# Kernel optimization log

Measured on AMD Instinct MI355X. Metric: run time of the kernel, lower is better.

Reference implementation:

```python
import jax, jax.numpy as jnp
import numpy as np

K_NB = 16
HID = 64
CIN = 128
EPS = 1e-5


def knn_idx(q, t, k):
    # q [B,N,3] queries, t [B,M,3] targets -> idx [B,N,k] into targets
    d = (jnp.sum(q * q, -1)[:, :, None] + jnp.sum(t * t, -1)[:, None, :]
         - 2.0 * jnp.einsum('bnd,bmd->bnm', q, t))
    _, idx = jax.lax.top_k(-d, k)
    return idx


def gather(feat, idx):
    # feat [B,C,M], idx [B,N,K] -> [B,C,N,K]
    return jax.vmap(lambda f, i: f[:, i])(feat, idx)


def conv1x1(x, W, b):
    # x [B,C,N,K], W [O,C], b [O]
    return jnp.einsum('oc,bcnk->bonk', W, x) + b[None, :, None, None]


def group_norm(x, gamma, beta, groups):
    B, C, N, K = x.shape
    xg = x.reshape(B, groups, C // groups, N, K)
    m = xg.mean(axis=(2, 3, 4), keepdims=True)
    v = xg.var(axis=(2, 3, 4), keepdims=True)
    xg = (xg - m) / jnp.sqrt(v + EPS)
    x = xg.reshape(B, C, N, K)
    return x * gamma[None, :, None, None] + beta[None, :, None, None]


def leaky(x):
    return jnp.where(x >= 0, x, 0.1 * x)


def setup_inputs() -> dict:
    key = jax.random.key(0)
    ks = jax.random.split(key, 20)
    B, N = 2, 4096
    d = {
        'xyz0': jax.random.normal(ks[0], (B, 3, N), jnp.float32),
        'xyz1': jax.random.normal(ks[1], (B, 3, N), jnp.float32),
        'state': jax.random.normal(ks[2], (B, HID, N), jnp.float32),
        'corr0': jax.random.normal(ks[3], (B, HID, N), jnp.float32),
        'feat0': jax.random.normal(ks[4], (B, CIN, N), jnp.float32),
        'feat1': jax.random.normal(ks[5], (B, CIN, N), jnp.float32),
        'flow0': jax.random.normal(ks[6], (B, 3, N), jnp.float32),
        # flow_layer: SetConv(3, [64,64]) -> convs take 3+3=6 then 64 in-chans
        'fw1': jax.random.normal(ks[7], (64, 6), jnp.float32) * 0.05,
        'fb1': jnp.zeros((64,), jnp.float32),
        'fg1': jnp.ones((64,), jnp.float32),
        'fbe1': jnp.zeros((64,), jnp.float32),
        'fw2': jax.random.normal(ks[8], (64, 64), jnp.float32) * 0.05,
        'fb2': jnp.zeros((64,), jnp.float32),
        'fg2': jnp.ones((64,), jnp.float32),
        'fbe2': jnp.zeros((64,), jnp.float32),
        # GRU gates: SetConv in_feat = hid(64)+(hid+64=128)=192, +3 = 195 -> 64, no act
        'wz': jax.random.normal(ks[9], (HID, 195), jnp.float32) * 0.05,
        'bz': jnp.zeros((HID,), jnp.float32),
        'wr': jax.random.normal(ks[10], (HID, 195), jnp.float32) * 0.05,
        'br': jnp.zeros((HID,), jnp.float32),
        'wq': jax.random.normal(ks[11], (HID, 195), jnp.float32) * 0.05,
        'bq': jnp.zeros((HID,), jnp.float32),
        # interp weight_net: 2*128+3=259 -> 128 -> 64
        'wa1': jax.random.normal(ks[12], (CIN, 2 * CIN + 3), jnp.float32) * 0.05,
        'ba1': jnp.zeros((CIN,), jnp.float32),
        'wa2': jax.random.normal(ks[13], (HID, CIN), jnp.float32) * 0.05,
        'ba2': jnp.zeros((HID,), jnp.float32),
    }
    return d


def reference(xyz0, xyz1, state, corr0, feat0, feat1, flow0,
              fw1, fb1, fg1, fbe1, fw2, fb2, fg2, fbe2,
              wz, bz, wr, br, wq, bq, wa1, ba1, wa2, ba2):
    xyz0_t = xyz0.transpose(0, 2, 1)  # [B,N,3]
    xyz1_t = xyz1.transpose(0, 2, 1)

    # ---- flow_layer: SetConv (KNN, N==npoint so new_xyz = xyz0) ----
    idx0 = knn_idx(xyz0_t, xyz0_t, K_NB)              # [B,N,K]
    gxyz0 = gather(xyz0, idx0) - xyz0[:, :, :, None]  # [B,3,N,K]
    h = jnp.concatenate([gather(flow0, idx0), gxyz0], axis=1)  # [B,6,N,K]
    h = leaky(group_norm(conv1x1(h, fw1, fb1), fg1, fbe1, 64 // 16))
    h = leaky(group_norm(conv1x1(h, fw2, fb2), fg2, fbe2, 64 // 16))
    flow_feat = h.max(axis=3)  # [B,64,N]

    # ---- iter_layer: SetGRU over xyz0 neighbors ----
    feat_g = jnp.concatenate([corr0, flow_feat], axis=1)  # [B,128,N]

    def gate(f, W, b):
        g = jnp.concatenate([gather(f, idx0), gxyz0], axis=1)
        return conv1x1(g, W, b).max(axis=3)  # [B,64,N]

    hid_in = jnp.concatenate([feat_g, state], axis=1)  # [B,192,N]
    z = jax.nn.sigmoid(gate(hid_in, wz, bz))
    r = jax.nn.sigmoid(gate(hid_in, wr, br))
    q = jnp.tanh(gate(jnp.concatenate([feat_g, r * state], axis=1), wq, bq))
    next_state = (1.0 - z) * state + z * q  # [B,64,N]

    # ---- align_layer: SetInterp (queries xyz1, targets xyz0) ----
    idx1 = knn_idx(xyz1_t, xyz0_t, K_NB)
    gv = gather(next_state, idx1)                        # [B,64,N,K]
    gx = gather(xyz0, idx1) - xyz1[:, :, :, None]        # [B,3,N,K]
    gf = jnp.concatenate([
        gather(feat0, idx1),
        jnp.broadcast_to(feat1[:, :, :, None], feat1.shape + (K_NB,))], axis=1)
    w = conv1x1(jnp.concatenate([gf, gx], axis=1), wa1, ba1)
    w = conv1x1(leaky(w), wa2, ba2)
    w = jax.nn.softmax(w, axis=3)
    return jnp.sum(gv * w, axis=3)  # [B,64,N]
```

## Files before the change

### kernel.cpp

```cpp
#include <hip/hip_runtime.h>

#define B_SZ 2

__device__ __forceinline__ int rfl(int x) { return __builtin_amdgcn_readfirstlane(x); }
__device__ __forceinline__ float leaky(float v) { return v >= 0.f ? v : 0.1f * v; }

__launch_bounds__(256)
__global__ void pack_kernel(const float* __restrict__ xyz, float4* __restrict__ out, int N)
{
  int b = blockIdx.y;
  int i = blockIdx.x * 256 + threadIdx.x;
  if (i >= N) return;
  const float* p = xyz + (size_t)b * 3 * N;
  float x = p[i], y = p[N + i], z = p[2 * N + i];
  out[(size_t)b * N + i] = make_float4(x, y, z, x * x + y * y + z * z);
}

__device__ __forceinline__ void sort64(float& d, int& i, int lane)
{
#pragma unroll
  for (int k = 2; k <= 64; k <<= 1) {
#pragma unroll
    for (int j = k >> 1; j > 0; j >>= 1) {
      float od = __shfl_xor(d, j, 64);
      int   oi = __shfl_xor(i, j, 64);
      bool mineSmall = (d < od) || (d == od && i < oi);
      bool amLow = (lane & j) == 0;
      bool up = (lane & k) == 0;
      bool keepMine = (amLow == up) ? mineSmall : !mineSmall;
      if (!keepMine) { d = od; i = oi; }
    }
  }
}

__launch_bounds__(256)
__global__ void knn_wave_kernel(const float4* __restrict__ pk, const float* __restrict__ q,
                                int* __restrict__ idx, int N)
{
  __shared__ __align__(16) float4 ts[1024];
  __shared__ uint2 buf[4][256];
  const int b = blockIdx.y;
  const int lane = threadIdx.x & 63, wav = rfl(threadIdx.x >> 6);
  const int qi = blockIdx.x * 4 + wav;
  const float* qb = q + (size_t)b * 3 * N;
  const float qx = qb[qi], qy = qb[N + qi], qz = qb[2 * N + qi];
  const float qq = qx * qx + qy * qy + qz * qz;
  const float4* pb = pk + (size_t)b * N;

  float lmin = 3.0e38f;
  for (int ch = 0; ch < N; ch += 1024) {
    __syncthreads();
    for (int i = threadIdx.x; i < 1024; i += 256) ts[i] = pb[ch + i];
    __syncthreads();
#pragma unroll 4
    for (int sub = 0; sub < 16; ++sub) {
      float4 v = ts[sub * 64 + lane];
      float key = (qq + v.w) - 2.0f * (qx * v.x + qy * v.y + qz * v.z);
      lmin = fminf(lmin, key);
    }
  }
  float gm = fminf(lmin, __shfl_xor(lmin, 1, 64));
  gm = fminf(gm, __shfl_xor(gm, 2, 64));
  float t0 = gm;
  t0 = fmaxf(t0, __shfl_xor(t0, 4, 64));
  t0 = fmaxf(t0, __shfl_xor(t0, 8, 64));
  t0 = fmaxf(t0, __shfl_xor(t0, 16, 64));
  t0 = fmaxf(t0, __shfl_xor(t0, 32, 64));

  int cnt = 0;
  for (int ch = 0; ch < N; ch += 1024) {
    __syncthreads();
    for (int i = threadIdx.x; i < 1024; i += 256) ts[i] = pb[ch + i];
    __syncthreads();
    for (int sub = 0; sub < 16; ++sub) {
      float4 v = ts[sub * 64 + lane];
      float key = (qq + v.w) - 2.0f * (qx * v.x + qy * v.y + qz * v.z);
      bool qf = key <= t0;
      unsigned long long mask = __ballot(qf);
      if (mask) {
        unsigned lo = __builtin_amdgcn_mbcnt_lo((unsigned)mask, 0u);
        unsigned pre = __builtin_amdgcn_mbcnt_hi((unsigned)(mask >> 32), lo);
        if (qf) {
          unsigned slot = (unsigned)cnt + pre;
          if (slot < 256u)
            buf[wav][slot] = make_uint2(__float_as_uint(key), (unsigned)(ch + sub * 64 + lane));
        }
        cnt += (int)__popcll(mask);
      }
    }
  }
  int C = cnt < 256 ? cnt : 256;

  float kd = 3.0e38f; int ki = 0x7fffffff;
  if (lane < C) { uint2 u = buf[wav][lane]; kd = __uint_as_float(u.x); ki = (int)u.y; }
  sort64(kd, ki, lane);
  int consumed = C < 64 ? C : 64;
  while (consumed < C) {
    if (lane >= 16) {
      int j2 = consumed + (lane - 16);
      if (j2 < C) { uint2 u = buf[wav][j2]; kd = __uint_as_float(u.x); ki = (int)u.y; }
      else { kd = 3.0e38f; ki = 0x7fffffff; }
    }
    int t = C - consumed; consumed += (t < 48 ? t : 48);
    sort64(kd, ki, lane);
  }
  if (lane < 16) idx[((size_t)b * N + qi) * 16 + lane] = ki;
}

__launch_bounds__(256)
__global__ void prep_w_kernel(const float* __restrict__ wz, const float* __restrict__ wr,
    const float* __restrict__ wq, const float* __restrict__ wa1, const float* __restrict__ wa2,
    const float* __restrict__ bz, const float* __restrict__ br,
    float* __restrict__ WtZR, float* __restrict__ WtQ,
    float* __restrict__ WtU, float* __restrict__ WtV, float* __restrict__ WtA2,
    float* __restrict__ bZR)
{
  int job = blockIdx.x;
  int tid = threadIdx.x;
  if (job == 0) {
    for (int e = tid; e < 195 * 128; e += 256) {
      int k = e >> 7, o = e & 127;
      const float* w = (o < 64) ? wz : wr;
      WtZR[(size_t)k * 128 + o] = w[(size_t)(o & 63) * 195 + k];
    }
    if (tid < 128) bZR[tid] = (tid < 64) ? bz[tid] : br[tid - 64];
  } else if (job == 1) {
    for (int e = tid; e < 195 * 64; e += 256) {
      int k = e >> 6, o = e & 63;
      WtQ[(size_t)k * 64 + o] = wq[(size_t)o * 195 + k];
    }
  } else if (job == 2) {
    for (int e = tid; e < 131 * 128; e += 256) {
      int k = e >> 7, o = e & 127;
      int col = (k < 128) ? k : 256 + (k - 128);
      WtU[(size_t)k * 128 + o] = wa1[(size_t)o * 259 + col];
    }
  } else if (job == 3) {
    for (int e = tid; e < 131 * 128; e += 256) {
      int k = e >> 7, o = e & 127;
      float v = (k < 128) ? wa1[(size_t)o * 259 + 128 + k]
                          : -wa1[(size_t)o * 259 + 256 + (k - 128)];
      WtV[(size_t)k * 128 + o] = v;
    }
  } else {
    for (int e = tid; e < 128 * 64; e += 256) {
      int c = e >> 6, o = e & 63;
      WtA2[e] = wa2[(size_t)o * 128 + c];
    }
  }
}

#define KC 66
__launch_bounds__(256)
__global__ void projT_kernel(const float* __restrict__ Wt, int K, int WOUT,
    const float* __restrict__ bias, float* __restrict__ out,
    int N, int PN,
    const float* __restrict__ s0, int c0, int l0,
    const float* __restrict__ s1, int c1, int l1,
    const float* __restrict__ s2, int c2, int l2,
    const float* __restrict__ s3, int c3, int l3)
{
  __shared__ __align__(16) float Ws[KC][68];
  __shared__ __align__(16) float Xs[KC][68];
  const int n0 = blockIdx.x * 64;
  const int oo = blockIdx.y * 64;
  const int b = n0 / N;
  const int nn0 = n0 - b * N;
  const int tid = threadIdx.x;
  const int tx = tid & 15, ty = tid >> 4;
  const int o4 = tx * 4, n4 = ty * 4;
  float acc[4][4];
#pragma unroll
  for (int i = 0; i < 4; ++i)
#pragma unroll
    for (int j = 0; j < 4; ++j)
      acc[i][j] = bias ? bias[oo + o4 + j] : 0.0f;

  const int e01 = c0 + c1, e012 = c0 + c1 + c2;
  for (int k0 = 0; k0 < K; k0 += KC) {
    const int kc = min(KC, K - k0);
    __syncthreads();
    for (int e = tid; e < kc * 64; e += 256) {
      int k = e >> 6, o = e & 63;
      Ws[k][o] = Wt[(size_t)(k0 + k) * WOUT + oo + o];
    }
    for (int e = tid; e < kc * 64; e += 256) {
      int k = e >> 6, j = e & 63;
      int c = k0 + k;
      float v;
      if (c < c0)        v = l0 ? s0[(size_t)c * PN + n0 + j]
                                : s0[((size_t)b * c0 + c) * N + nn0 + j];
      else if (c < e01)  { int cc = c - c0;
                           v = l1 ? s1[(size_t)cc * PN + n0 + j]
                                  : s1[((size_t)b * c1 + cc) * N + nn0 + j]; }
      else if (c < e012) { int cc = c - e01;
                           v = l2 ? s2[(size_t)cc * PN + n0 + j]
                                  : s2[((size_t)b * c2 + cc) * N + nn0 + j]; }
      else               { int cc = c - e012;
                           v = l3 ? s3[(size_t)cc * PN + n0 + j]
                                  : s3[((size_t)b * c3 + cc) * N + nn0 + j]; }
      Xs[k][j] = v;
    }
    __syncthreads();
#pragma unroll 2
    for (int k = 0; k < kc; ++k) {
      float4 wv = *(const float4*)&Ws[k][o4];
      float4 xv = *(const float4*)&Xs[k][n4];
      acc[0][0] = fmaf(xv.x, wv.x, acc[0][0]); acc[0][1] = fmaf(xv.x, wv.y, acc[0][1]);
      acc[0][2] = fmaf(xv.x, wv.z, acc[0][2]); acc[0][3] = fmaf(xv.x, wv.w, acc[0][3]);
      acc[1][0] = fmaf(xv.y, wv.x, acc[1][0]); acc[1][1] = fmaf(xv.y, wv.y, acc[1][1]);
      acc[1][2] = fmaf(xv.y, wv.z, acc[1][2]); acc[1][3] = fmaf(xv.y, wv.w, acc[1][3]);
      acc[2][0] = fmaf(xv.z, wv.x, acc[2][0]); acc[2][1] = fmaf(xv.z, wv.y, acc[2][1]);
      acc[2][2] = fmaf(xv.z, wv.z, acc[2][2]); acc[2][3] = fmaf(xv.z, wv.w, acc[2][3]);
      acc[3][0] = fmaf(xv.w, wv.x, acc[3][0]); acc[3][1] = fmaf(xv.w, wv.y, acc[3][1]);
      acc[3][2] = fmaf(xv.w, wv.z, acc[3][2]); acc[3][3] = fmaf(xv.w, wv.w, acc[3][3]);
    }
  }
#pragma unroll
  for (int i = 0; i < 4; ++i) {
    float4 r = make_float4(acc[i][0], acc[i][1], acc[i][2], acc[i][3]);
    *(float4*)&out[(size_t)(n0 + n4 + i) * WOUT + oo + o4] = r;
  }
}

__launch_bounds__(256)
__global__ void projUV_kernel(const float* __restrict__ WtU, const float* __restrict__ WtV,
    const float* __restrict__ ba1, float* __restrict__ Uo, float* __restrict__ Vo,
    int N, int PN,
    const float* __restrict__ feat0, const float* __restrict__ feat1,
    const float* __restrict__ x0, const float* __restrict__ x1)
{
  __shared__ __align__(16) float Ws[KC][68];
  __shared__ __align__(16) float Xs[KC][68];
  const int z = blockIdx.z;
  const float* Wt = z ? WtV : WtU;
  const float* bias = z ? ba1 : 0;
  float* out = z ? Vo : Uo;
  const float* s0 = z ? feat1 : feat0;
  const float* s1 = z ? x1 : x0;
  const int K = 131, WOUT = 128, c0 = 128;
  const int n0 = blockIdx.x * 64;
  const int oo = blockIdx.y * 64;
  const int b = n0 / N;
  const int nn0 = n0 - b * N;
  const int tid = threadIdx.x;
  const int tx = tid & 15, ty = tid >> 4;
  const int o4 = tx * 4, n4 = ty * 4;
  float acc[4][4];
#pragma unroll
  for (int i = 0; i < 4; ++i)
#pragma unroll
    for (int j = 0; j < 4; ++j)
      acc[i][j] = bias ? bias[oo + o4 + j] : 0.0f;

  for (int k0 = 0; k0 < K; k0 += KC) {
    const int kc = min(KC, K - k0);
    __syncthreads();
    for (int e = tid; e < kc * 64; e += 256) {
      int k = e >> 6, o = e & 63;
      Ws[k][o] = Wt[(size_t)(k0 + k) * WOUT + oo + o];
    }
    for (int e = tid; e < kc * 64; e += 256) {
      int k = e >> 6, j = e & 63;
      int c = k0 + k;
      float v;
      if (c < c0) v = s0[((size_t)b * c0 + c) * N + nn0 + j];
      else        v = s1[((size_t)b * 3 + (c - c0)) * N + nn0 + j];
      Xs[k][j] = v;
    }
    __syncthreads();
#pragma unroll 2
    for (int k = 0; k < kc; ++k) {
      float4 wv = *(const float4*)&Ws[k][o4];
      float4 xv = *(const float4*)&Xs[k][n4];
      acc[0][0] = fmaf(xv.x, wv.x, acc[0][0]); acc[0][1] = fmaf(xv.x, wv.y, acc[0][1]);
      acc[0][2] = fmaf(xv.x, wv.z, acc[0][2]); acc[0][3] = fmaf(xv.x, wv.w, acc[0][3]);
      acc[1][0] = fmaf(xv.y, wv.x, acc[1][0]); acc[1][1] = fmaf(xv.y, wv.y, acc[1][1]);
      acc[1][2] = fmaf(xv.y, wv.z, acc[1][2]); acc[1][3] = fmaf(xv.y, wv.w, acc[1][3]);
      acc[2][0] = fmaf(xv.z, wv.x, acc[2][0]); acc[2][1] = fmaf(xv.z, wv.y, acc[2][1]);
      acc[2][2] = fmaf(xv.z, wv.z, acc[2][2]); acc[2][3] = fmaf(xv.z, wv.w, acc[2][3]);
      acc[3][0] = fmaf(xv.w, wv.x, acc[3][0]); acc[3][1] = fmaf(xv.w, wv.y, acc[3][1]);
      acc[3][2] = fmaf(xv.w, wv.z, acc[3][2]); acc[3][3] = fmaf(xv.w, wv.w, acc[3][3]);
    }
  }
#pragma unroll
  for (int i = 0; i < 4; ++i) {
    float4 r = make_float4(acc[i][0], acc[i][1], acc[i][2], acc[i][3]);
    *(float4*)&out[(size_t)(n0 + n4 + i) * WOUT + oo + o4] = r;
  }
}

__device__ __forceinline__ void seg_accumL(const float* __restrict__ p, int cnt,
    const float* __restrict__ WL, int sC, int sN, long n0, float acc[4])
{
#pragma unroll 4
  for (int c = 0; c < cnt; ++c) {
    float w = WL[c];
    const float* pp = p + (size_t)c * sC + (size_t)n0 * sN;
#pragma unroll
    for (int m = 0; m < 4; ++m)
      acc[m] = fmaf(w, pp[(size_t)m * sN], acc[m]);
  }
}

template<int WP>
__launch_bounds__(256)
__global__ void proj_kernel(
    const float* __restrict__ W0, const float* __restrict__ bias,
    float* __restrict__ out, int OUTS, int wld, int N,
    const float* __restrict__ s0, int c0, int w0,
    const float* __restrict__ s1, int c1, int w1)
{
  __shared__ float Wl[64 * WP];
  const int b = blockIdx.y;
  const int lane = threadIdx.x & 63;
  const int wav = rfl(threadIdx.x >> 6);
  for (int r = wav; r < 64; r += 4)
    for (int c = lane; c < c0; c += 64)
      Wl[r * WP + c] = W0[(size_t)r * wld + w0 + c];
  for (int r = wav; r < 64; r += 4)
    for (int c = lane; c < c1; c += 64)
      Wl[r * WP + c0 + c] = W0[(size_t)r * wld + w1 + c];
  __syncthreads();
  const long n0 = ((long)blockIdx.x * 4 + wav) * 4;
  float bv = bias ? bias[lane] : 0.0f;
  float acc[4] = {bv, bv, bv, bv};
  const float* WL = &Wl[lane * WP];
  seg_accumL(s0 + (size_t)b * c0 * N, c0, WL, N, 1, n0, acc);
  seg_accumL(s1 + (size_t)b * c1 * N, c1, WL + c0, N, 1, n0, acc);
#pragma unroll
  for (int m = 0; m < 4; ++m)
    out[((size_t)b * N + n0 + m) * OUTS + lane] = acc[m];
}

__launch_bounds__(256)
__global__ void gn1_stats_kernel(const float* __restrict__ G1, const float* __restrict__ xyz0,
    const float* __restrict__ fw1, const int* __restrict__ idx0,
    float* __restrict__ stats1, int N)
{
  __shared__ float red[4][4][2];
  int b = blockIdx.y;
  int lane = threadIdx.x & 63, wav = rfl(threadIdx.x >> 6);
  float wg0 = fw1[lane * 6 + 3], wg1 = fw1[lane * 6 + 4], wg2 = fw1[lane * 6 + 5];
  const float* xb = xyz0 + (size_t)b * 3 * N;
  float sum = 0.f, sq = 0.f;
  for (int n = blockIdx.x * 4 + wav; n < N; n += gridDim.x * 4) {
    const int* ip = idx0 + ((size_t)b * N + n) * 16;
    float bx = wg0 * xb[n] + wg1 * xb[N + n] + wg2 * xb[2 * N + n];
#pragma unroll
    for (int k = 0; k < 16; ++k) {
      int m = ip[k];
      float y = G1[((size_t)b * N + m) * 64 + lane] - bx;
      sum += y; sq += y * y;
    }
  }
#pragma unroll
  for (int off = 1; off < 16; off <<= 1) {
    sum += __shfl_xor(sum, off, 64);
    sq += __shfl_xor(sq, off, 64);
  }
  int g = lane >> 4;
  if ((lane & 15) == 0) { red[wav][g][0] = sum; red[wav][g][1] = sq; }
  __syncthreads();
  if (threadIdx.x < 8) {
    int gg = threadIdx.x >> 1, s = threadIdx.x & 1;
    float v = red[0][gg][s] + red[1][gg][s] + red[2][gg][s] + red[3][gg][s];
    atomicAdd(&stats1[(b * 4 + gg) * 2 + s], v);
  }
}

__launch_bounds__(256, 2)
__global__ void conv2_kernel(const float* __restrict__ G1, const float* __restrict__ xyz0,
    const float* __restrict__ fw1, const int* __restrict__ idx0,
    const float* __restrict__ fw2, const float* __restrict__ fb2,
    const float* __restrict__ fg1, const float* __restrict__ fbe1,
    const float* __restrict__ raw1, float cnt,
    float* __restrict__ y2max, float* __restrict__ y2min,
    float* __restrict__ stats2, int N)
{
  __shared__ __align__(16) float x2[4][16][64];
  __shared__ float red[4][4][2];
  const int b = blockIdx.y;
  const int lane = threadIdx.x & 63;
  const int wav = rfl(threadIdx.x >> 6);
  float4 w[16];
#pragma unroll
  for (int i = 0; i < 16; ++i) w[i] = *(const float4*)&fw2[lane * 64 + i * 4];
  float wg0 = fw1[lane * 6 + 3], wg1 = fw1[lane * 6 + 4], wg2 = fw1[lane * 6 + 5];
  const int g = lane >> 4;
  float s_ = raw1[(b * 4 + g) * 2], q_ = raw1[(b * 4 + g) * 2 + 1];
  float mu1 = s_ / cnt;
  float inv1 = rsqrtf(q_ / cnt - mu1 * mu1 + 1e-5f);
  float sc1 = fg1[lane] * inv1;
  float sh1 = fbe1[lane] - mu1 * sc1;
  float fb2l = fb2[lane];
  const float* xb = xyz0 + (size_t)b * 3 * N;
  float sum = 0.f, sq = 0.f;
  for (int n = blockIdx.x * 4 + wav; n < N; n += gridDim.x * 4) {
    const int* ip = idx0 + ((size_t)b * N + n) * 16;
    float bx = wg0 * xb[n] + wg1 * xb[N + n] + wg2 * xb[2 * N + n];
#pragma unroll
    for (int k = 0; k < 16; ++k) {
      int m = ip[k];
      float y = G1[((size_t)b * N + m) * 64 + lane] - bx;
      x2[wav][k][lane] = leaky(y * sc1 + sh1);
    }
    float acc[16];
#pragma unroll
    for (int k = 0; k < 16; ++k) acc[k] = fb2l;
#pragma unroll
    for (int c4 = 0; c4 < 16; ++c4) {
      float4 w4 = w[c4];
#pragma unroll
      for (int k = 0; k < 16; ++k) {
        float4 x4 = *(const float4*)&x2[wav][k][c4 * 4];
        acc[k] = fmaf(w4.x, x4.x, acc[k]);
        acc[k] = fmaf(w4.y, x4.y, acc[k]);
        acc[k] = fmaf(w4.z, x4.z, acc[k]);
        acc[k] = fmaf(w4.w, x4.w, acc[k]);
      }
    }
    float mx = -3.0e38f, mn = 3.0e38f;
#pragma unroll
    for (int k = 0; k < 16; ++k) {
      mx = fmaxf(mx, acc[k]); mn = fminf(mn, acc[k]);
      sum += acc[k]; sq += acc[k] * acc[k];
    }
    y2max[((size_t)b * N + n) * 64 + lane] = mx;
    y2min[((size_t)b * N + n) * 64 + lane] = mn;
  }
#pragma unroll
  for (int off = 1; off < 16; off <<= 1) {
    sum += __shfl_xor(sum, off, 64);
    sq += __shfl_xor(sq, off, 64);
  }
  if ((lane & 15) == 0) { red[wav][g][0] = sum; red[wav][g][1] = sq; }
  __syncthreads();
  if (threadIdx.x < 8) {
    int gg = threadIdx.x >> 1, s = threadIdx.x & 1;
    float v = red[0][gg][s] + red[1][gg][s] + red[2][gg][s] + red[3][gg][s];
    atomicAdd(&stats2[(b * 4 + gg) * 2 + s], v);
  }
}

__launch_bounds__(256)
__global__ void flow_feat_kernel(const float* __restrict__ y2max, const float* __restrict__ y2min,
    const float* __restrict__ raw2, float cnt,
    const float* __restrict__ fg2, const float* __restrict__ fbe2,
    float* __restrict__ ff_t, int N, int PN)
{
  size_t i = (size_t)blockIdx.x * blockDim.x + threadIdx.x;
  if (i >= (size_t)B_SZ * N * 64) return;
  int c = i & 63;
  size_t pn = i >> 6;
  int b = (int)(pn / N);
  int g = c >> 4;
  float s_ = raw2[(b * 4 + g) * 2], q_ = raw2[(b * 4 + g) * 2 + 1];
  float mu = s_ / cnt;
  float inv = rsqrtf(q_ / cnt - mu * mu + 1e-5f);
  float sc = fg2[c] * inv;
  float sh = fbe2[c] - mu * sc;
  float y = (sc >= 0.0f) ? y2max[i] : y2min[i];
  ff_t[(size_t)c * PN + pn] = leaky(y * sc + sh);
}

__launch_bounds__(256)
__global__ void gate_zr_kernel(const float* __restrict__ Szr,
    const float* __restrict__ wz, const float* __restrict__ wr,
    const float* __restrict__ xyz0, const float* __restrict__ state,
    const int* __restrict__ idx0,
    float* __restrict__ zo, float* __restrict__ rs_t, int N, int PN)
{
  int b = blockIdx.y;
  int lane = threadIdx.x & 63, wav = rfl(threadIdx.x >> 6);
  float wz0 = wz[lane * 195 + 192], wz1 = wz[lane * 195 + 193], wz2 = wz[lane * 195 + 194];
  float wr0 = wr[lane * 195 + 192], wr1 = wr[lane * 195 + 193], wr2 = wr[lane * 195 + 194];
  const float* xb = xyz0 + (size_t)b * 3 * N;
  for (int n = blockIdx.x * 4 + wav; n < N; n += gridDim.x * 4) {
    const int* ip = idx0 + ((size_t)b * N + n) * 16;
    float u0 = xb[n], u1 = xb[N + n], u2 = xb[2 * N + n];
    float xz = wz0 * u0 + wz1 * u1 + wz2 * u2;
    float xr = wr0 * u0 + wr1 * u1 + wr2 * u2;
    float mz = -3.0e38f, mr = -3.0e38f;
#pragma unroll
    for (int k = 0; k < 16; ++k) {
      size_t mo = ((size_t)b * N + ip[k]) * 128 + lane;
      mz = fmaxf(mz, Szr[mo]);
      mr = fmaxf(mr, Szr[mo + 64]);
    }
    size_t no = ((size_t)b * N + n) * 64 + lane;
    float z = 1.f / (1.f + expf(-(mz - xz)));
    float r = 1.f / (1.f + expf(-(mr - xr)));
    zo[no] = z;
    rs_t[(size_t)lane * PN + (size_t)b * N + n] = r * state[((size_t)b * 64 + lane) * N + n];
  }
}

__launch_bounds__(256)
__global__ void gate_q_ns_kernel(const float* __restrict__ Sq, const float* __restrict__ wq,
    const float* __restrict__ xyz0, const float* __restrict__ zo,
    const float* __restrict__ state, const int* __restrict__ idx0,
    float* __restrict__ ns, int N)
{
  int b = blockIdx.y;
  int lane = threadIdx.x & 63, wav = rfl(threadIdx.x >> 6);
  float wq0 = wq[lane * 195 + 192], wq1 = wq[lane * 195 + 193], wq2 = wq[lane * 195 + 194];
  const float* xb = xyz0 + (size_t)b * 3 * N;
  for (int n = blockIdx.x * 4 + wav; n < N; n += gridDim.x * 4) {
    const int* ip = idx0 + ((size_t)b * N + n) * 16;
    float xq = wq0 * xb[n] + wq1 * xb[N + n] + wq2 * xb[2 * N + n];
    float mq = -3.0e38f;
#pragma unroll
    for (int k = 0; k < 16; ++k)
      mq = fmaxf(mq, Sq[((size_t)b * N + ip[k]) * 64 + lane]);
    size_t no = ((size_t)b * N + n) * 64 + lane;
    float q = tanhf(mq - xq);
    float z = zo[no];
    float st = state[((size_t)b * 64 + lane) * N + n];
    ns[no] = (1.f - z) * st + z * q;
  }
}

__launch_bounds__(256, 2)
__global__ void align_kernel(const float* __restrict__ U, const float* __restrict__ V,
    const float* __restrict__ WtA2, const float* __restrict__ ba2,
    const float* __restrict__ ns, const int* __restrict__ idx1,
    float* __restrict__ out, int N)
{
  __shared__ __align__(16) float Xs[64][128];
  __shared__ __align__(16) float Ws[128][64];
  const int b = blockIdx.y;
  const int tid = threadIdx.x;
  const int lane = tid & 63;
  const int wav = rfl(tid >> 6);

  for (int e = tid; e < 2048; e += 256) {
    int c = e >> 4, o4 = (e & 15) << 2;
    *(float4*)&Ws[c][o4] = *(const float4*)&WtA2[(c << 6) + o4];
  }

  const int n = blockIdx.x * 4 + wav;
  int mkreg = 0;
  {
    const int* ip = idx1 + ((size_t)b * N + n) * 16;
    if (lane < 16) mkreg = ip[lane];
  }
  const int c4l = lane & 31;
  const int half = lane >> 5;
  float4 v4 = *(const float4*)&V[(((size_t)b * N + n) << 7) + (c4l << 2)];
  for (int k0 = 0; k0 < 16; k0 += 2) {
    int k = k0 + half;
    int m = __shfl(mkreg, k);
    float4 u4 = *(const float4*)&U[(((size_t)b * N + m) << 7) + (c4l << 2)];
    float4 xv;
    xv.x = leaky(u4.x + v4.x);
    xv.y = leaky(u4.y + v4.y);
    xv.z = leaky(u4.z + v4.z);
    xv.w = leaky(u4.w + v4.w);
    int row = (wav << 4) + k;
    *(float4*)&Xs[row][(c4l ^ (row & 7)) << 2] = xv;
  }
  __syncthreads();

  const int tx = tid & 15, ty = tid >> 4;
  const int o4 = tx << 2, r0 = ty << 2;
  float4 bav = *(const float4*)&ba2[o4];
  float acc[4][4];
#pragma unroll
  for (int i = 0; i < 4; ++i) {
    acc[i][0] = bav.x; acc[i][1] = bav.y; acc[i][2] = bav.z; acc[i][3] = bav.w;
  }
  for (int c4 = 0; c4 < 32; ++c4) {
    float4 wv0 = *(const float4*)&Ws[c4 * 4 + 0][o4];
    float4 wv1 = *(const float4*)&Ws[c4 * 4 + 1][o4];
    float4 wv2 = *(const float4*)&Ws[c4 * 4 + 2][o4];
    float4 wv3 = *(const float4*)&Ws[c4 * 4 + 3][o4];
#pragma unroll
    for (int i = 0; i < 4; ++i) {
      int row = r0 + i;
      float4 xv = *(const float4*)&Xs[row][(c4 ^ (row & 7)) << 2];
      acc[i][0] = fmaf(xv.x, wv0.x, acc[i][0]);
      acc[i][1] = fmaf(xv.x, wv0.y, acc[i][1]);
      acc[i][2] = fmaf(xv.x, wv0.z, acc[i][2]);
      acc[i][3] = fmaf(xv.x, wv0.w, acc[i][3]);
      acc[i][0] = fmaf(xv.y, wv1.x, acc[i][0]);
      acc[i][1] = fmaf(xv.y, wv1.y, acc[i][1]);
      acc[i][2] = fmaf(xv.y, wv1.z, acc[i][2]);
      acc[i][3] = fmaf(xv.y, wv1.w, acc[i][3]);
      acc[i][0] = fmaf(xv.z, wv2.x, acc[i][0]);
      acc[i][1] = fmaf(xv.z, wv2.y, acc[i][1]);
      acc[i][2] = fmaf(xv.z, wv2.z, acc[i][2]);
      acc[i][3] = fmaf(xv.z, wv2.w, acc[i][3]);
      acc[i][0] = fmaf(xv.w, wv3.x, acc[i][0]);
      acc[i][1] = fmaf(xv.w, wv3.y, acc[i][1]);
      acc[i][2] = fmaf(xv.w, wv3.z, acc[i][2]);
      acc[i][3] = fmaf(xv.w, wv3.w, acc[i][3]);
    }
  }

  float m_[4];
#pragma unroll
  for (int j = 0; j < 4; ++j) {
    float m = fmaxf(fmaxf(acc[0][j], acc[1][j]), fmaxf(acc[2][j], acc[3][j]));
    m = fmaxf(m, __shfl_xor(m, 16, 64));
    m = fmaxf(m, __shfl_xor(m, 32, 64));
    m_[j] = m;
  }
  float e_[4][4], s_[4];
#pragma unroll
  for (int j = 0; j < 4; ++j) {
    float s = 0.f;
#pragma unroll
    for (int i = 0; i < 4; ++i) { e_[i][j] = expf(acc[i][j] - m_[j]); s += e_[i][j]; }
    s += __shfl_xor(s, 16, 64);
    s += __shfl_xor(s, 32, 64);
    s_[j] = s;
  }
  float o_[4] = {0.f, 0.f, 0.f, 0.f};
#pragma unroll
  for (int i = 0; i < 4; ++i) {
    int k = (r0 + i) & 15;
    int m = __shfl(mkreg, k);
    float4 nsv = *(const float4*)&ns[(((size_t)b * N + m) << 6) + o4];
    o_[0] = fmaf(e_[i][0], nsv.x, o_[0]);
    o_[1] = fmaf(e_[i][1], nsv.y, o_[1]);
    o_[2] = fmaf(e_[i][2], nsv.z, o_[2]);
    o_[3] = fmaf(e_[i][3], nsv.w, o_[3]);
  }
#pragma unroll
  for (int j = 0; j < 4; ++j) {
    o_[j] += __shfl_xor(o_[j], 16, 64);
    o_[j] += __shfl_xor(o_[j], 32, 64);
  }
  if ((lane >> 4) == 0) {
#pragma unroll
    for (int j = 0; j < 4; ++j)
      out[((size_t)b * 64 + o4 + j) * N + n] = o_[j] / s_[j];
  }
}

extern "C" void kernel_launch(void* const* d_in, const int* in_sizes, int n_in,
                              void* d_out, int out_size, void* d_ws, size_t ws_size,
                              hipStream_t stream) {
  (void)n_in; (void)out_size; (void)ws_size;
  const float* xyz0 = (const float*)d_in[0];
  const float* xyz1 = (const float*)d_in[1];
  const float* state = (const float*)d_in[2];
  const float* corr0 = (const float*)d_in[3];
  const float* feat0 = (const float*)d_in[4];
  const float* feat1 = (const float*)d_in[5];
  const float* flow0 = (const float*)d_in[6];
  const float* fw1 = (const float*)d_in[7];
  const float* fb1 = (const float*)d_in[8];
  const float* fg1 = (const float*)d_in[9];
  const float* fbe1 = (const float*)d_in[10];
  const float* fw2 = (const float*)d_in[11];
  const float* fb2 = (const float*)d_in[12];
  const float* fg2 = (const float*)d_in[13];
  const float* fbe2 = (const float*)d_in[14];
  const float* wz = (const float*)d_in[15];
  const float* bz = (const float*)d_in[16];
  const float* wr = (const float*)d_in[17];
  const float* br = (const float*)d_in[18];
  const float* wq = (const float*)d_in[19];
  const float* bq = (const float*)d_in[20];
  const float* wa1 = (const float*)d_in[21];
  const float* ba1 = (const float*)d_in[22];
  const float* wa2 = (const float*)d_in[23];
  const float* ba2 = (const float*)d_in[24];
  float* out = (float*)d_out;

  const int N = in_sizes[0] / (3 * B_SZ);
  const int PN = B_SZ * N;
  char* wsb = (char*)d_ws;
  size_t off = 0;
  auto take = [&](size_t bytes) -> char* {
    char* p = wsb + off;
    off += (bytes + 255) & ~(size_t)255;
    return p;
  };
  float* U    = (float*)take((size_t)PN * 128 * 4);
  float* V    = (float*)take((size_t)PN * 128 * 4);
  float* Szr  = (float*)take((size_t)PN * 128 * 4);
  float4* pk0 = (float4*)take((size_t)PN * 4 * 4);
  int*   idx0 = (int*)  take((size_t)PN * 16 * 4);
  int*   idx1 = (int*)  take((size_t)PN * 16 * 4);
  float* G1   = (float*)take((size_t)PN * 64 * 4);
  float* y2mx = (float*)take((size_t)PN * 64 * 4);
  float* y2mn = (float*)take((size_t)PN * 64 * 4);
  float* ff_t = (float*)take((size_t)PN * 64 * 4);
  float* Sq   = (float*)take((size_t)PN * 64 * 4);
  float* zg   = (float*)take((size_t)PN * 64 * 4);
  float* rs_t = (float*)take((size_t)PN * 64 * 4);
  float* ns   = (float*)take((size_t)PN * 64 * 4);
  float* WtZR = (float*)take(195 * 128 * 4);
  float* WtQ  = (float*)take(195 * 64 * 4);
  float* WtU  = (float*)take(131 * 128 * 4);
  float* WtV  = (float*)take(131 * 128 * 4);
  float* WtA2 = (float*)take(128 * 64 * 4);
  float* bZR  = (float*)take(128 * 4);
  float* stats = (float*)take(256);
  float* raw1 = stats, *raw2 = stats + 16;

  const float cntv = 16.0f * N * 16.0f;

  hipMemsetAsync(raw1, 0, 32 * sizeof(float), stream);

  pack_kernel<<<dim3((N + 255) / 256, B_SZ), 256, 0, stream>>>(xyz0, pk0, N);
  prep_w_kernel<<<5, 256, 0, stream>>>(wz, wr, wq, wa1, wa2, bz, br,
      WtZR, WtQ, WtU, WtV, WtA2, bZR);
  knn_wave_kernel<<<dim3(N / 4, B_SZ), 256, 0, stream>>>(pk0, xyz0, idx0, N);
  knn_wave_kernel<<<dim3(N / 4, B_SZ), 256, 0, stream>>>(pk0, xyz1, idx1, N);

  proj_kernel<7><<<dim3(N / 16, B_SZ), 256, 0, stream>>>(
      fw1, fb1, G1, 64, 6, N, flow0, 3, 0, xyz0, 3, 3);

  gn1_stats_kernel<<<dim3(256, B_SZ), 256, 0, stream>>>(G1, xyz0, fw1, idx0, raw1, N);
  conv2_kernel<<<dim3(512, B_SZ), 256, 0, stream>>>(G1, xyz0, fw1, idx0, fw2, fb2, fg1, fbe1,
      raw1, cntv, y2mx, y2mn, raw2, N);
  flow_feat_kernel<<<dim3((unsigned)((size_t)PN * 64 / 256)), 256, 0, stream>>>(
      y2mx, y2mn, raw2, cntv, fg2, fbe2, ff_t, N, PN);

  projT_kernel<<<dim3(PN / 64, 2), 256, 0, stream>>>(WtZR, 195, 128, bZR, Szr, N, PN,
      corr0, 64, 0,  ff_t, 64, 1,  state, 64, 0,  xyz0, 3, 0);

  gate_zr_kernel<<<dim3(256, B_SZ), 256, 0, stream>>>(Szr, wz, wr, xyz0, state, idx0, zg, rs_t, N, PN);

  projT_kernel<<<dim3(PN / 64, 1), 256, 0, stream>>>(WtQ, 195, 64, bq, Sq, N, PN,
      corr0, 64, 0,  ff_t, 64, 1,  rs_t, 64, 1,  xyz0, 3, 0);

  gate_q_ns_kernel<<<dim3(256, B_SZ), 256, 0, stream>>>(Sq, wq, xyz0, zg, state, idx0, ns, N);

  projUV_kernel<<<dim3(PN / 64, 2, 2), 256, 0, stream>>>(WtU, WtV, ba1, U, V, N, PN,
      feat0, feat1, xyz0, xyz1);

  align_kernel<<<dim3(N / 4, B_SZ), 256, 0, stream>>>(U, V, WtA2, ba2, ns, idx1, out, N);
}
```

Baseline: 337.8 us.

## Fuse both kNN searches into one launch with four queries per wave

Merges the two kNN launches into one kernel covering both query sets. Each wave now handles four queries instead of one, so every target point staged in shared memory is reused across four distance computations. This cuts global-to-LDS staging traffic and barrier count per query and removes one launch. In exchange it raises register and LDS use (the candidate buffer grows fourfold to 32KB), which may lower occupancy, and the per-query ballot and sort work is now serialized within each wave.

```diff
diff --git a/kernel.cpp b/kernel.cpp
--- a/kernel.cpp
+++ b/kernel.cpp
@@ -34,77 +34,101 @@
 }
 
 __launch_bounds__(256)
-__global__ void knn_wave_kernel(const float4* __restrict__ pk, const float* __restrict__ q,
-                                int* __restrict__ idx, int N)
+__global__ void knn_fused_kernel(const float4* __restrict__ pk,
+    const float* __restrict__ q0, const float* __restrict__ q1,
+    int* __restrict__ idx0, int* __restrict__ idx1, int N, int PN)
 {
   __shared__ __align__(16) float4 ts[1024];
-  __shared__ uint2 buf[4][256];
-  const int b = blockIdx.y;
+  __shared__ uint2 buf[4][4][256];
   const int lane = threadIdx.x & 63, wav = rfl(threadIdx.x >> 6);
-  const int qi = blockIdx.x * 4 + wav;
-  const float* qb = q + (size_t)b * 3 * N;
-  const float qx = qb[qi], qy = qb[N + qi], qz = qb[2 * N + qi];
-  const float qq = qx * qx + qy * qy + qz * qz;
+  const int qg0 = blockIdx.x * 16 + wav * 4;
+  const bool src1 = qg0 >= PN;
+  const int qloc0 = src1 ? (qg0 - PN) : qg0;
+  const int b = qloc0 / N;
+  const int n0 = qloc0 - b * N;
+  const float* qb = (src1 ? q1 : q0) + (size_t)b * 3 * N;
+
+  float qx[4], qy[4], qz[4], qq[4], lmin[4];
+#pragma unroll
+  for (int j = 0; j < 4; ++j) {
+    qx[j] = qb[n0 + j]; qy[j] = qb[N + n0 + j]; qz[j] = qb[2 * N + n0 + j];
+    qq[j] = qx[j] * qx[j] + qy[j] * qy[j] + qz[j] * qz[j];
+    lmin[j] = 3.0e38f;
+  }
   const float4* pb = pk + (size_t)b * N;
 
-  float lmin = 3.0e38f;
-  for (int ch = 0; ch < N; ch += 1024) {
-    __syncthreads();
-    for (int i = threadIdx.x; i < 1024; i += 256) ts[i] = pb[ch + i];
-    __syncthreads();
-#pragma unroll 4
-    for (int sub = 0; sub < 16; ++sub) {
-      float4 v = ts[sub * 64 + lane];
-      float key = (qq + v.w) - 2.0f * (qx * v.x + qy * v.y + qz * v.z);
-      lmin = fminf(lmin, key);
-    }
-  }
-  float gm = fminf(lmin, __shfl_xor(lmin, 1, 64));
-  gm = fminf(gm, __shfl_xor(gm, 2, 64));
-  float t0 = gm;
-  t0 = fmaxf(t0, __shfl_xor(t0, 4, 64));
-  t0 = fmaxf(t0, __shfl_xor(t0, 8, 64));
-  t0 = fmaxf(t0, __shfl_xor(t0, 16, 64));
-  t0 = fmaxf(t0, __shfl_xor(t0, 32, 64));
-
-  int cnt = 0;
   for (int ch = 0; ch < N; ch += 1024) {
     __syncthreads();
     for (int i = threadIdx.x; i < 1024; i += 256) ts[i] = pb[ch + i];
     __syncthreads();
     for (int sub = 0; sub < 16; ++sub) {
       float4 v = ts[sub * 64 + lane];
-      float key = (qq + v.w) - 2.0f * (qx * v.x + qy * v.y + qz * v.z);
-      bool qf = key <= t0;
-      unsigned long long mask = __ballot(qf);
-      if (mask) {
-        unsigned lo = __builtin_amdgcn_mbcnt_lo((unsigned)mask, 0u);
-        unsigned pre = __builtin_amdgcn_mbcnt_hi((unsigned)(mask >> 32), lo);
-        if (qf) {
-          unsigned slot = (unsigned)cnt + pre;
-          if (slot < 256u)
-            buf[wav][slot] = make_uint2(__float_as_uint(key), (unsigned)(ch + sub * 64 + lane));
+#pragma unroll
+      for (int j = 0; j < 4; ++j) {
+        float key = (qq[j] + v.w) - 2.0f * (qx[j] * v.x + qy[j] * v.y + qz[j] * v.z);
+        lmin[j] = fminf(lmin[j], key);
+      }
+    }
+  }
+  float t0[4];
+#pragma unroll
+  for (int j = 0; j < 4; ++j) {
+    float gm = fminf(lmin[j], __shfl_xor(lmin[j], 1, 64));
+    gm = fminf(gm, __shfl_xor(gm, 2, 64));
+    float t = gm;
+    t = fmaxf(t, __shfl_xor(t, 4, 64));
+    t = fmaxf(t, __shfl_xor(t, 8, 64));
+    t = fmaxf(t, __shfl_xor(t, 16, 64));
+    t = fmaxf(t, __shfl_xor(t, 32, 64));
+    t0[j] = t;
+  }
+
+  int cnt[4] = {0, 0, 0, 0};
+  for (int ch = 0; ch < N; ch += 1024) {
+    __syncthreads();
+    for (int i = threadIdx.x; i < 1024; i += 256) ts[i] = pb[ch + i];
+    __syncthreads();
+    for (int sub = 0; sub < 16; ++sub) {
+      float4 v = ts[sub * 64 + lane];
+#pragma unroll
+      for (int j = 0; j < 4; ++j) {
+        float key = (qq[j] + v.w) - 2.0f * (qx[j] * v.x + qy[j] * v.y + qz[j] * v.z);
+        bool qf = key <= t0[j];
+        unsigned long long mask = __ballot(qf);
+        if (mask) {
+          unsigned lo = __builtin_amdgcn_mbcnt_lo((unsigned)mask, 0u);
+          unsigned pre = __builtin_amdgcn_mbcnt_hi((unsigned)(mask >> 32), lo);
+          if (qf) {
+            unsigned slot = (unsigned)cnt[j] + pre;
+            if (slot < 256u)
+              buf[wav][j][slot] = make_uint2(__float_as_uint(key),
+                                             (unsigned)(ch + sub * 64 + lane));
+          }
+          cnt[j] += (int)__popcll(mask);
         }
-        cnt += (int)__popcll(mask);
       }
     }
   }
-  int C = cnt < 256 ? cnt : 256;
-
-  float kd = 3.0e38f; int ki = 0x7fffffff;
-  if (lane < C) { uint2 u = buf[wav][lane]; kd = __uint_as_float(u.x); ki = (int)u.y; }
-  sort64(kd, ki, lane);
-  int consumed = C < 64 ? C : 64;
-  while (consumed < C) {
-    if (lane >= 16) {
-      int j2 = consumed + (lane - 16);
-      if (j2 < C) { uint2 u = buf[wav][j2]; kd = __uint_as_float(u.x); ki = (int)u.y; }
-      else { kd = 3.0e38f; ki = 0x7fffffff; }
-    }
-    int t = C - consumed; consumed += (t < 48 ? t : 48);
+
+  int* op = src1 ? idx1 : idx0;
+#pragma unroll
+  for (int j = 0; j < 4; ++j) {
+    int C = cnt[j] < 256 ? cnt[j] : 256;
+    float kd = 3.0e38f; int ki = 0x7fffffff;
+    if (lane < C) { uint2 u = buf[wav][j][lane]; kd = __uint_as_float(u.x); ki = (int)u.y; }
     sort64(kd, ki, lane);
-  }
-  if (lane < 16) idx[((size_t)b * N + qi) * 16 + lane] = ki;
+    int consumed = C < 64 ? C : 64;
+    while (consumed < C) {
+      if (lane >= 16) {
+        int j2 = consumed + (lane - 16);
+        if (j2 < C) { uint2 u = buf[wav][j][j2]; kd = __uint_as_float(u.x); ki = (int)u.y; }
+        else { kd = 3.0e38f; ki = 0x7fffffff; }
+      }
+      int t = C - consumed; consumed += (t < 48 ? t : 48);
+      sort64(kd, ki, lane);
+    }
+    if (lane < 16) op[((size_t)b * N + n0 + j) * 16 + lane] = ki;
+  }
 }
 
 __launch_bounds__(256)
@@ -709,8 +733,7 @@
   pack_kernel<<<dim3((N + 255) / 256, B_SZ), 256, 0, stream>>>(xyz0, pk0, N);
   prep_w_kernel<<<5, 256, 0, stream>>>(wz, wr, wq, wa1, wa2, bz, br,
       WtZR, WtQ, WtU, WtV, WtA2, bZR);
-  knn_wave_kernel<<<dim3(N / 4, B_SZ), 256, 0, stream>>>(pk0, xyz0, idx0, N);
-  knn_wave_kernel<<<dim3(N / 4, B_SZ), 256, 0, stream>>>(pk0, xyz1, idx1, N);
+  knn_fused_kernel<<<dim3(2 * PN / 16), 256, 0, stream>>>(pk0, xyz0, xyz1, idx0, idx1, N, PN);
 
   proj_kernel<7><<<dim3(N / 16, B_SZ), 256, 0, stream>>>(
       fw1, fb1, G1, 64, 6, N, flow0, 3, 0, xyz0, 3, 3);
```

Result: no change. 339.2 us (+0.4%).
